# Kernel tuning notes

Measured on AMD Instinct MI355X. Metric: run time of the kernel, lower is better.

The kernel has to match this reference:

```python
import jax, jax.numpy as jnp
import numpy as np

N_NODES = 50000
N_EDGES = 600000
N_MOL = 512
N_ATOM_FEAT = 30   # NUMBER_ATOMIC_GRAPH_FEATURES
N_BOND_FEAT = 10   # NUMBER_BOND_GRAPH_FEATURES


def _sh(v):
    # Real solid spherical harmonics l=0..3, e3nn 'component' normalization
    # (sum_m Y_lm^2 = (2l+1) r^{2l}), normalize=False -> homogeneous polynomials.
    x, y, z = v[..., 0], v[..., 1], v[..., 2]
    r2 = x * x + y * y + z * z
    s3, s5, s15, s105 = 3 ** 0.5, 5 ** 0.5, 15 ** 0.5, 105 ** 0.5
    s70_4, s42_4, s7_2, s105_2 = 70 ** 0.5 / 4, 42 ** 0.5 / 4, 7 ** 0.5 / 2, 105 ** 0.5 / 2
    return jnp.stack([
        jnp.ones_like(x),                                               # l=0
        s3 * x, s3 * y, s3 * z,                                         # l=1
        s15 * x * y, s15 * y * z, 0.5 * s5 * (3 * z * z - r2),
        s15 * x * z, 0.5 * s15 * (x * x - y * y),                       # l=2
        s70_4 * y * (3 * x * x - y * y), s105 * x * y * z,
        s42_4 * y * (5 * z * z - r2), s7_2 * z * (5 * z * z - 3 * r2),
        s42_4 * x * (5 * z * z - r2), s105_2 * z * (x * x - y * y),
        s70_4 * x * (x * x - 3 * y * y),                                # l=3 (no TP path uses it)
    ], axis=-1)


def setup_inputs() -> dict:
    key = jax.random.key(0)
    ks = jax.random.split(key, 12)
    positions = jax.random.normal(ks[0], (N_NODES, 3), jnp.float32)
    x = jax.random.normal(ks[1], (N_NODES, N_ATOM_FEAT), jnp.float32)
    edge_attr = jax.random.normal(ks[2], (N_EDGES, N_BOND_FEAT), jnp.float32)
    edge_src = jax.random.randint(ks[3], (N_EDGES,), 0, N_NODES)
    edge_dst = jax.random.randint(ks[4], (N_EDGES,), 0, N_NODES)
    batch = jnp.sort(jax.random.randint(ks[5], (N_NODES,), 0, N_MOL))
    # tp1: FullyConnectedTensorProduct(30x0e, sh) -> live outputs 64x0e + 24x1o + 16x2e
    W1_0 = jax.random.normal(ks[6], (N_ATOM_FEAT, 64), jnp.float32)
    W1_1 = jax.random.normal(ks[7], (N_ATOM_FEAT, 24), jnp.float32)
    W1_2 = jax.random.normal(ks[8], (N_ATOM_FEAT, 16), jnp.float32)
    # tp2: paths 0e*0e, 1o*1o, 2e*2e -> 1x0e
    W2_0 = jax.random.normal(ks[9], (64,), jnp.float32)
    W2_1 = jax.random.normal(ks[10], (24,), jnp.float32)
    W2_2 = jax.random.normal(ks[11], (16,), jnp.float32)
    return dict(positions=positions, x=x, edge_attr=edge_attr,
                W1_0=W1_0, W1_1=W1_1, W1_2=W1_2,
                W2_0=W2_0, W2_1=W2_1, W2_2=W2_2,
                edge_src=edge_src, edge_dst=edge_dst, batch=batch)


def _forward(positions, x, edge_attr, W1_0, W1_1, W1_2, W2_0, W2_1, W2_2,
             edge_src, edge_dst, batch):
    E = edge_src.shape[0]
    seg = jax.ops.segment_sum
    edge_vec = positions[edge_src] - positions[edge_dst]            # [E,3]
    sh = _sh(edge_vec)                                              # [E,16]
    # mul_edges TP: only bond channel 0 has instructions; path_weight sqrt(2l+1)
    # cancels w3j(0,l,l)=I/sqrt(2l+1) exactly -> plain product.
    ea = edge_attr[:, :1] * sh
    ea0, ea1, ea2 = ea[:, 0:1], ea[:, 1:4], ea[:, 4:9]              # l=3 slice unused (no path)
    deg = seg(jnp.ones((E,), sh.dtype), edge_dst, num_segments=N_NODES)
    inv_sqrt_deg = jnp.where(deg > 0, jax.lax.rsqrt(jnp.maximum(deg, 1.0)), 0.0)[:, None]
    # tp1: 0e x l -> l ; path_weight*w3j collapses to 1/sqrt(fan_in=30)
    W1 = jnp.concatenate([W1_0, W1_1, W1_2], axis=1)                # [30,104]
    a = (x[edge_src] @ W1) * (1.0 / np.sqrt(N_ATOM_FEAT))           # [E,104]
    a0, a1, a2 = a[:, :64], a[:, 64:88], a[:, 88:104]
    e_feat = jnp.concatenate([
        a0 * ea0,                                                   # [E,64]  0e
        (a1[:, :, None] * ea1[:, None, :]).reshape(E, 72),          # [E,24*3] 1o
        (a2[:, :, None] * ea2[:, None, :]).reshape(E, 80),          # [E,16*5] 2e
    ], axis=1)                                                      # [E,216]
    n = seg(e_feat, edge_dst, num_segments=N_NODES) * inv_sqrt_deg  # [N,216]
    # tp2: l x l -> 0e, w3j(l,l,0)=I/sqrt(2l+1), path_weight = 1/sqrt(104)
    g = n[edge_src]                                                 # [E,216]
    t0 = (g[:, :64] * ea0) @ W2_0
    t1 = jnp.einsum('eum,em,u->e', g[:, 64:136].reshape(E, 24, 3), ea1, W2_1)
    t2 = jnp.einsum('eum,em,u->e', g[:, 136:216].reshape(E, 16, 5), ea2, W2_2)
    out_e = (t0 + t1 / np.sqrt(3.0) + t2 / np.sqrt(5.0)) * (1.0 / np.sqrt(104.0))
    node = seg(out_e[:, None], edge_dst, num_segments=N_NODES) * inv_sqrt_deg  # [N,1]
    acc = seg(node, batch, num_segments=N_MOL)                      # [M,1]
    atoms = seg(jnp.ones((N_NODES,), node.dtype), batch, num_segments=N_MOL)[:, None]
    return acc * jnp.where(atoms > 0, jax.lax.rsqrt(jnp.maximum(atoms, 1.0)), 0.0)


def reference(positions, x, edge_attr, W1_0, W1_1, W1_2, W2_0, W2_1, W2_2,
              edge_src, edge_dst, batch):
    return _forward(positions, x, edge_attr, W1_0, W1_1, W1_2,
                    W2_0, W2_1, W2_2, edge_src, edge_dst, batch)
```

## Files before the change

kernel.cpp:

```cpp
#include <hip/hip_runtime.h>

#define DEV_INLINE __device__ __forceinline__
#define MAXDEG 64

static DEV_INLINE void sh_l012(float xx, float yy, float zz, float sh[9]) {
    const float s3  = 1.7320508075688772f;
    const float s5  = 2.23606797749979f;
    const float s15 = 3.872983346207417f;
    float r2 = xx * xx + yy * yy + zz * zz;
    sh[0] = 1.0f;
    sh[1] = s3 * xx;
    sh[2] = s3 * yy;
    sh[3] = s3 * zz;
    sh[4] = s15 * xx * yy;
    sh[5] = s15 * yy * zz;
    sh[6] = 0.5f * s5 * (3.0f * zz * zz - r2);
    sh[7] = s15 * xx * zz;
    sh[8] = 0.5f * s15 * (xx * xx - yy * yy);
}

__global__ void k_prep(const float* __restrict__ x,
                       const float* __restrict__ pos,
                       const float* __restrict__ W1_0, const float* __restrict__ W1_1,
                       const float* __restrict__ W1_2, const float* __restrict__ W2_0,
                       const float* __restrict__ W2_1, const float* __restrict__ W2_2,
                       const int* __restrict__ esrc, const int* __restrict__ edst,
                       const float* __restrict__ eattr, const int* __restrict__ batch,
                       float4* __restrict__ node1, float2* __restrict__ node2,
                       int* __restrict__ deg, int2* __restrict__ rec,
                       int* __restrict__ atoms,
                       int n_nodes, int n_edges) {
    __shared__ float ws[90];
    __shared__ int hist[512];
    int t = threadIdx.x;
    int g = blockIdx.x * blockDim.x + t;
    bool nodeBlock = (blockIdx.x * blockDim.x) < n_nodes;
    if (nodeBlock) {
        const float inv_s30 = 0.18257418583505536f;
        if (t < 30) {
            float s = 0.f;
            for (int u = 0; u < 64; u++) s += W1_0[t * 64 + u] * W2_0[u];
            ws[t] = s * inv_s30;
        } else if (t < 60) {
            int k = t - 30;
            float s = 0.f;
            for (int u = 0; u < 24; u++) s += W1_1[k * 24 + u] * W2_1[u];
            ws[t] = s * inv_s30;
        } else if (t < 90) {
            int k = t - 60;
            float s = 0.f;
            for (int u = 0; u < 16; u++) s += W1_2[k * 16 + u] * W2_2[u];
            ws[t] = s * inv_s30;
        }
        hist[t] = 0;
        hist[t + 256] = 0;
        __syncthreads();
        if (g < n_nodes) {
            const float* xv = x + (size_t)g * 30;
            float s0 = 0.f, s1 = 0.f, s2 = 0.f;
#pragma unroll
            for (int k = 0; k < 30; k++) {
                float xk = xv[k];
                s0 += xk * ws[k];
                s1 += xk * ws[30 + k];
                s2 += xk * ws[60 + k];
            }
            node1[g] = make_float4(pos[g * 3 + 0], pos[g * 3 + 1], pos[g * 3 + 2], s0);
            node2[g] = make_float2(s1, s2);
        }
        int v0 = blockIdx.x * 256;
        int molFirst = batch[min(v0, n_nodes - 1)];
        if (g < n_nodes) atomicAdd(&hist[batch[g] - molFirst], 1);
        __syncthreads();
        int vend = min(v0 + 255, n_nodes - 1);
        int molLast = batch[vend];
        for (int m = t; m <= molLast - molFirst; m += 256)
            if (hist[m] > 0) atomicAdd(atoms + molFirst + m, hist[m]);
    }
    int e = 4 * g;
    if (e + 3 < n_edges) {
        int4 d4 = ((const int4*)edst)[g];
        int4 s4 = ((const int4*)esrc)[g];
        float ea0 = eattr[(size_t)(e + 0) * 10];
        float ea1 = eattr[(size_t)(e + 1) * 10];
        float ea2 = eattr[(size_t)(e + 2) * 10];
        float ea3 = eattr[(size_t)(e + 3) * 10];
        int r0 = atomicAdd(deg + d4.x, 1);
        int r1 = atomicAdd(deg + d4.y, 1);
        int r2 = atomicAdd(deg + d4.z, 1);
        int r3 = atomicAdd(deg + d4.w, 1);
        if (r0 < MAXDEG) rec[d4.x * MAXDEG + r0] = make_int2(s4.x, __float_as_int(ea0));
        if (r1 < MAXDEG) rec[d4.y * MAXDEG + r1] = make_int2(s4.y, __float_as_int(ea1));
        if (r2 < MAXDEG) rec[d4.z * MAXDEG + r2] = make_int2(s4.z, __float_as_int(ea2));
        if (r3 < MAXDEG) rec[d4.w * MAXDEG + r3] = make_int2(s4.w, __float_as_int(ea3));
    } else {
        for (int ee = e; ee < n_edges; ee++) {
            int dst = edst[ee];
            int r = atomicAdd(deg + dst, 1);
            if (r < MAXDEG)
                rec[dst * MAXDEG + r] = make_int2(esrc[ee], __float_as_int(eattr[(size_t)ee * 10]));
        }
    }
}

__global__ void k_passA(const float4* __restrict__ node1, const float2* __restrict__ node2,
                        const int2* __restrict__ rec, const int* __restrict__ deg,
                        float4* __restrict__ Pkg, int n_nodes) {
    int g = blockIdx.x * blockDim.x + threadIdx.x;
    int v = g >> 4, r = g & 15;
    if (v >= n_nodes) return;
    int d = min(deg[v], MAXDEG);
    const int2* row = rec + (size_t)v * MAXDEG;
    float4 pv = node1[v];
    float acc[9];
#pragma unroll
    for (int m = 0; m < 9; m++) acc[m] = 0.f;
    for (int i = r; i < d; i += 16) {
        int2 rcd = row[i];
        int src = rcd.x;
        float ea = __int_as_float(rcd.y);
        float4 n1 = node1[src];
        float2 n2 = node2[src];
        float dx = n1.x - pv.x, dy = n1.y - pv.y, dz = n1.z - pv.z;
        float sh[9];
        sh_l012(dx, dy, dz, sh);
        acc[0] += ea * n1.w;
#pragma unroll
        for (int m = 1; m < 4; m++) acc[m] += ea * sh[m] * n2.x;
#pragma unroll
        for (int m = 4; m < 9; m++) acc[m] += ea * sh[m] * n2.y;
    }
#pragma unroll
    for (int off = 1; off < 16; off <<= 1)
#pragma unroll
        for (int m = 0; m < 9; m++) acc[m] += __shfl_xor(acc[m], off);
    if (r == 0) {
        float s = (d > 0) ? rsqrtf((float)d) : 0.f;
        float4* out = Pkg + (size_t)v * 3;
        out[0] = make_float4(acc[0] * s, acc[1] * s, acc[2] * s, acc[3] * s);
        out[1] = make_float4(acc[4] * s, acc[5] * s, acc[6] * s, acc[7] * s);
        out[2] = make_float4(acc[8] * s, pv.x, pv.y, pv.z);
    }
}

__global__ void k_passB(const float4* __restrict__ node1, const float4* __restrict__ Pkg,
                        const int2* __restrict__ rec, const int* __restrict__ deg,
                        const int* __restrict__ batch, const int* __restrict__ atoms,
                        float* __restrict__ out, int n_nodes) {
    __shared__ float smol[512];
    int t = threadIdx.x;
    smol[t] = 0.f;
    smol[t + 256] = 0.f;
    __syncthreads();
    int g = blockIdx.x * blockDim.x + t;
    int v = g >> 4, r = g & 15;
    int v0 = blockIdx.x * 16;
    const float i3 = 0.5773502691896258f;
    const float i5 = 0.4472135954999579f;
    const float i104 = 0.09805806756909202f;
    int molFirst = batch[min(v0, n_nodes - 1)];
    if (v < n_nodes) {
        int d = min(deg[v], MAXDEG);
        const int2* row = rec + (size_t)v * MAXDEG;
        float4 pv = node1[v];
        float s = 0.f;
        for (int i = r; i < d; i += 16) {
            int2 rcd = row[i];
            int src = rcd.x;
            float ea = __int_as_float(rcd.y);
            const float4* Ps = Pkg + (size_t)src * 3;
            float4 p03 = Ps[0];
            float4 p47 = Ps[1];
            float4 p8p = Ps[2];
            float dx = p8p.y - pv.x, dy = p8p.z - pv.y, dz = p8p.w - pv.z;
            float sh[9];
            sh_l012(dx, dy, dz, sh);
            float t1 = sh[1] * p03.y + sh[2] * p03.z + sh[3] * p03.w;
            float t2 = sh[4] * p47.x + sh[5] * p47.y + sh[6] * p47.z + sh[7] * p47.w + sh[8] * p8p.x;
            s += ea * (p03.x + t1 * i3 + t2 * i5);
        }
#pragma unroll
        for (int off = 1; off < 16; off <<= 1) s += __shfl_xor(s, off);
        if (r == 0) {
            float isd = (d > 0) ? rsqrtf((float)d) : 0.f;
            atomicAdd(&smol[batch[v] - molFirst], s * i104 * isd);
        }
    }
    __syncthreads();
    if (v0 < n_nodes) {
        int vend = min(v0 + 15, n_nodes - 1);
        int nm = batch[vend] - molFirst + 1;
        for (int m = t; m < nm; m += 256) {
            float val = smol[m];
            if (val != 0.f) {
                int a = atoms[molFirst + m];
                float inv = (a > 0) ? rsqrtf((float)a) : 0.f;
                atomicAdd(out + molFirst + m, val * inv);
            }
        }
    }
}

extern "C" void kernel_launch(void* const* d_in, const int* in_sizes, int n_in,
                              void* d_out, int out_size, void* d_ws, size_t ws_size,
                              hipStream_t stream) {
    const float* pos   = (const float*)d_in[0];
    const float* x     = (const float*)d_in[1];
    const float* eattr = (const float*)d_in[2];
    const float* W1_0  = (const float*)d_in[3];
    const float* W1_1  = (const float*)d_in[4];
    const float* W1_2  = (const float*)d_in[5];
    const float* W2_0  = (const float*)d_in[6];
    const float* W2_1  = (const float*)d_in[7];
    const float* W2_2  = (const float*)d_in[8];
    const int* esrc  = (const int*)d_in[9];
    const int* edst  = (const int*)d_in[10];
    const int* batch = (const int*)d_in[11];

    const int n_edges = in_sizes[9];
    const int n_nodes = in_sizes[11];
    const int n_mol   = out_size;
    float* out = (float*)d_out;

    const int BS = 256;
    const int NB = (n_nodes + BS - 1) / BS;
    const int EB4 = (n_edges / 4 + BS - 1) / BS;
    const int VB16 = (16 * n_nodes + BS - 1) / BS;
    const int GRID1 = (EB4 > NB) ? EB4 : NB;

    char* ws = (char*)d_ws;
    size_t off = 0;
    auto carve = [&](size_t bytes) {
        size_t o = off;
        off = (off + bytes + 255) & ~(size_t)255;
        return o;
    };
    size_t off_deg    = carve((size_t)n_nodes * sizeof(int));
    size_t off_atoms  = carve((size_t)n_mol * sizeof(int));
    size_t zero_bytes = off;
    size_t off_n1     = carve((size_t)n_nodes * sizeof(float4));
    size_t off_n2     = carve((size_t)n_nodes * sizeof(float2));
    size_t off_Pkg    = carve((size_t)n_nodes * 3 * sizeof(float4));
    size_t off_rec    = carve((size_t)n_nodes * MAXDEG * sizeof(int2));
    (void)ws_size;

    int*    deg    = (int*)(ws + off_deg);
    int*    atoms  = (int*)(ws + off_atoms);
    float4* node1  = (float4*)(ws + off_n1);
    float2* node2  = (float2*)(ws + off_n2);
    float4* Pkg    = (float4*)(ws + off_Pkg);
    int2*   rec    = (int2*)(ws + off_rec);

    hipMemsetAsync(d_ws, 0, zero_bytes, stream);
    hipMemsetAsync(d_out, 0, (size_t)n_mol * sizeof(float), stream);

    k_prep<<<GRID1, BS, 0, stream>>>(x, pos, W1_0, W1_1, W1_2, W2_0, W2_1, W2_2,
                                     esrc, edst, eattr, batch,
                                     node1, node2, deg, rec, atoms,
                                     n_nodes, n_edges);
    k_passA<<<VB16, BS, 0, stream>>>(node1, node2, rec, deg, Pkg, n_nodes);
    k_passB<<<VB16, BS, 0, stream>>>(node1, Pkg, rec, deg, batch, atoms, out, n_nodes);
}
```

Baseline: 152.9 us.

## Fuse prep and both edge passes into one cooperative kernel with grid syncs

Merges the prep, pass A and pass B kernels, and the two memsets, into a single cooperative kernel. It launches 1024 blocks of 256 threads, and the later phases become grid-stride loops over node chunks. Zeroing of deg, atoms and out moves inside the kernel, and grid-wide barriers replace the kernel boundaries. The goal is to remove launch and memset overhead and the idle gaps between stages. The cost is three grid.sync barriers and a fixed grid size that must fit co-resident on the device, which may also reduce per-phase occupancy.

```diff
diff --git a/kernel.cpp b/kernel.cpp
--- a/kernel.cpp
+++ b/kernel.cpp
@@ -1,4 +1,7 @@
 #include <hip/hip_runtime.h>
+#include <hip/hip_cooperative_groups.h>
+
+namespace cg = cooperative_groups;
 
 #define DEV_INLINE __device__ __forceinline__
 #define MAXDEG 64
@@ -19,21 +22,29 @@
     sh[8] = 0.5f * s15 * (xx * xx - yy * yy);
 }
 
-__global__ void k_prep(const float* __restrict__ x,
-                       const float* __restrict__ pos,
-                       const float* __restrict__ W1_0, const float* __restrict__ W1_1,
-                       const float* __restrict__ W1_2, const float* __restrict__ W2_0,
-                       const float* __restrict__ W2_1, const float* __restrict__ W2_2,
-                       const int* __restrict__ esrc, const int* __restrict__ edst,
-                       const float* __restrict__ eattr, const int* __restrict__ batch,
-                       float4* __restrict__ node1, float2* __restrict__ node2,
-                       int* __restrict__ deg, int2* __restrict__ rec,
-                       int* __restrict__ atoms,
-                       int n_nodes, int n_edges) {
+__global__ void __launch_bounds__(256, 4)
+k_all(const float* __restrict__ x, const float* __restrict__ pos,
+      const float* __restrict__ W1_0, const float* __restrict__ W1_1,
+      const float* __restrict__ W1_2, const float* __restrict__ W2_0,
+      const float* __restrict__ W2_1, const float* __restrict__ W2_2,
+      const int* __restrict__ esrc, const int* __restrict__ edst,
+      const float* __restrict__ eattr, const int* __restrict__ batch,
+      float4* __restrict__ node1, float2* __restrict__ node2,
+      int* __restrict__ deg, int2* __restrict__ rec, int* __restrict__ atoms,
+      float4* __restrict__ Pkg, float* __restrict__ out,
+      int n_nodes, int n_edges, int n_mol) {
+    cg::grid_group grid = cg::this_grid();
     __shared__ float ws[90];
     __shared__ int hist[512];
+    __shared__ float smol[512];
     int t = threadIdx.x;
     int g = blockIdx.x * blockDim.x + t;
+    int nthreads = gridDim.x * blockDim.x;
+
+    for (int i = g; i < n_nodes; i += nthreads) deg[i] = 0;
+    if (g < n_mol) { atoms[g] = 0; out[g] = 0.f; }
+    grid.sync();
+
     bool nodeBlock = (blockIdx.x * blockDim.x) < n_nodes;
     if (nodeBlock) {
         const float inv_s30 = 0.18257418583505536f;
@@ -77,127 +88,129 @@
         for (int m = t; m <= molLast - molFirst; m += 256)
             if (hist[m] > 0) atomicAdd(atoms + molFirst + m, hist[m]);
     }
-    int e = 4 * g;
-    if (e + 3 < n_edges) {
-        int4 d4 = ((const int4*)edst)[g];
-        int4 s4 = ((const int4*)esrc)[g];
-        float ea0 = eattr[(size_t)(e + 0) * 10];
-        float ea1 = eattr[(size_t)(e + 1) * 10];
-        float ea2 = eattr[(size_t)(e + 2) * 10];
-        float ea3 = eattr[(size_t)(e + 3) * 10];
-        int r0 = atomicAdd(deg + d4.x, 1);
-        int r1 = atomicAdd(deg + d4.y, 1);
-        int r2 = atomicAdd(deg + d4.z, 1);
-        int r3 = atomicAdd(deg + d4.w, 1);
-        if (r0 < MAXDEG) rec[d4.x * MAXDEG + r0] = make_int2(s4.x, __float_as_int(ea0));
-        if (r1 < MAXDEG) rec[d4.y * MAXDEG + r1] = make_int2(s4.y, __float_as_int(ea1));
-        if (r2 < MAXDEG) rec[d4.z * MAXDEG + r2] = make_int2(s4.z, __float_as_int(ea2));
-        if (r3 < MAXDEG) rec[d4.w * MAXDEG + r3] = make_int2(s4.w, __float_as_int(ea3));
-    } else {
-        for (int ee = e; ee < n_edges; ee++) {
-            int dst = edst[ee];
-            int r = atomicAdd(deg + dst, 1);
-            if (r < MAXDEG)
-                rec[dst * MAXDEG + r] = make_int2(esrc[ee], __float_as_int(eattr[(size_t)ee * 10]));
-        }
-    }
-}
-
-__global__ void k_passA(const float4* __restrict__ node1, const float2* __restrict__ node2,
-                        const int2* __restrict__ rec, const int* __restrict__ deg,
-                        float4* __restrict__ Pkg, int n_nodes) {
-    int g = blockIdx.x * blockDim.x + threadIdx.x;
-    int v = g >> 4, r = g & 15;
-    if (v >= n_nodes) return;
-    int d = min(deg[v], MAXDEG);
-    const int2* row = rec + (size_t)v * MAXDEG;
-    float4 pv = node1[v];
-    float acc[9];
-#pragma unroll
-    for (int m = 0; m < 9; m++) acc[m] = 0.f;
-    for (int i = r; i < d; i += 16) {
-        int2 rcd = row[i];
-        int src = rcd.x;
-        float ea = __int_as_float(rcd.y);
-        float4 n1 = node1[src];
-        float2 n2 = node2[src];
-        float dx = n1.x - pv.x, dy = n1.y - pv.y, dz = n1.z - pv.z;
-        float sh[9];
-        sh_l012(dx, dy, dz, sh);
-        acc[0] += ea * n1.w;
-#pragma unroll
-        for (int m = 1; m < 4; m++) acc[m] += ea * sh[m] * n2.x;
-#pragma unroll
-        for (int m = 4; m < 9; m++) acc[m] += ea * sh[m] * n2.y;
-    }
-#pragma unroll
-    for (int off = 1; off < 16; off <<= 1)
-#pragma unroll
-        for (int m = 0; m < 9; m++) acc[m] += __shfl_xor(acc[m], off);
-    if (r == 0) {
-        float s = (d > 0) ? rsqrtf((float)d) : 0.f;
-        float4* out = Pkg + (size_t)v * 3;
-        out[0] = make_float4(acc[0] * s, acc[1] * s, acc[2] * s, acc[3] * s);
-        out[1] = make_float4(acc[4] * s, acc[5] * s, acc[6] * s, acc[7] * s);
-        out[2] = make_float4(acc[8] * s, pv.x, pv.y, pv.z);
-    }
-}
-
-__global__ void k_passB(const float4* __restrict__ node1, const float4* __restrict__ Pkg,
-                        const int2* __restrict__ rec, const int* __restrict__ deg,
-                        const int* __restrict__ batch, const int* __restrict__ atoms,
-                        float* __restrict__ out, int n_nodes) {
-    __shared__ float smol[512];
-    int t = threadIdx.x;
-    smol[t] = 0.f;
-    smol[t + 256] = 0.f;
-    __syncthreads();
-    int g = blockIdx.x * blockDim.x + t;
-    int v = g >> 4, r = g & 15;
-    int v0 = blockIdx.x * 16;
+    {
+        int e = 4 * g;
+        if (e + 3 < n_edges) {
+            int4 d4 = ((const int4*)edst)[g];
+            int4 s4 = ((const int4*)esrc)[g];
+            float ea0 = eattr[(size_t)(e + 0) * 10];
+            float ea1 = eattr[(size_t)(e + 1) * 10];
+            float ea2 = eattr[(size_t)(e + 2) * 10];
+            float ea3 = eattr[(size_t)(e + 3) * 10];
+            int r0 = atomicAdd(deg + d4.x, 1);
+            int r1 = atomicAdd(deg + d4.y, 1);
+            int r2 = atomicAdd(deg + d4.z, 1);
+            int r3 = atomicAdd(deg + d4.w, 1);
+            if (r0 < MAXDEG) rec[d4.x * MAXDEG + r0] = make_int2(s4.x, __float_as_int(ea0));
+            if (r1 < MAXDEG) rec[d4.y * MAXDEG + r1] = make_int2(s4.y, __float_as_int(ea1));
+            if (r2 < MAXDEG) rec[d4.z * MAXDEG + r2] = make_int2(s4.z, __float_as_int(ea2));
+            if (r3 < MAXDEG) rec[d4.w * MAXDEG + r3] = make_int2(s4.w, __float_as_int(ea3));
+        } else {
+            for (int ee = e; ee < n_edges; ee++) {
+                int dst = edst[ee];
+                int r = atomicAdd(deg + dst, 1);
+                if (r < MAXDEG)
+                    rec[dst * MAXDEG + r] =
+                        make_int2(esrc[ee], __float_as_int(eattr[(size_t)ee * 10]));
+            }
+        }
+    }
+    grid.sync();
+
+    int nchunk = (16 * n_nodes + 255) / 256;
+    for (int c = blockIdx.x; c < nchunk; c += gridDim.x) {
+        int gg = c * 256 + t;
+        int v = gg >> 4, r = gg & 15;
+        if (v < n_nodes) {
+            int d = min(deg[v], MAXDEG);
+            const int2* row = rec + (size_t)v * MAXDEG;
+            float4 pv = node1[v];
+            float acc[9];
+#pragma unroll
+            for (int m = 0; m < 9; m++) acc[m] = 0.f;
+            for (int i = r; i < d; i += 16) {
+                int2 rcd = row[i];
+                int src = rcd.x;
+                float ea = __int_as_float(rcd.y);
+                float4 n1 = node1[src];
+                float2 n2 = node2[src];
+                float dx = n1.x - pv.x, dy = n1.y - pv.y, dz = n1.z - pv.z;
+                float sh[9];
+                sh_l012(dx, dy, dz, sh);
+                acc[0] += ea * n1.w;
+#pragma unroll
+                for (int m = 1; m < 4; m++) acc[m] += ea * sh[m] * n2.x;
+#pragma unroll
+                for (int m = 4; m < 9; m++) acc[m] += ea * sh[m] * n2.y;
+            }
+#pragma unroll
+            for (int off = 1; off < 16; off <<= 1)
+#pragma unroll
+                for (int m = 0; m < 9; m++) acc[m] += __shfl_xor(acc[m], off);
+            if (r == 0) {
+                float s = (d > 0) ? rsqrtf((float)d) : 0.f;
+                float4* o = Pkg + (size_t)v * 3;
+                o[0] = make_float4(acc[0] * s, acc[1] * s, acc[2] * s, acc[3] * s);
+                o[1] = make_float4(acc[4] * s, acc[5] * s, acc[6] * s, acc[7] * s);
+                o[2] = make_float4(acc[8] * s, pv.x, pv.y, pv.z);
+            }
+        }
+    }
+    grid.sync();
+
     const float i3 = 0.5773502691896258f;
     const float i5 = 0.4472135954999579f;
     const float i104 = 0.09805806756909202f;
-    int molFirst = batch[min(v0, n_nodes - 1)];
-    if (v < n_nodes) {
-        int d = min(deg[v], MAXDEG);
-        const int2* row = rec + (size_t)v * MAXDEG;
-        float4 pv = node1[v];
-        float s = 0.f;
-        for (int i = r; i < d; i += 16) {
-            int2 rcd = row[i];
-            int src = rcd.x;
-            float ea = __int_as_float(rcd.y);
-            const float4* Ps = Pkg + (size_t)src * 3;
-            float4 p03 = Ps[0];
-            float4 p47 = Ps[1];
-            float4 p8p = Ps[2];
-            float dx = p8p.y - pv.x, dy = p8p.z - pv.y, dz = p8p.w - pv.z;
-            float sh[9];
-            sh_l012(dx, dy, dz, sh);
-            float t1 = sh[1] * p03.y + sh[2] * p03.z + sh[3] * p03.w;
-            float t2 = sh[4] * p47.x + sh[5] * p47.y + sh[6] * p47.z + sh[7] * p47.w + sh[8] * p8p.x;
-            s += ea * (p03.x + t1 * i3 + t2 * i5);
-        }
-#pragma unroll
-        for (int off = 1; off < 16; off <<= 1) s += __shfl_xor(s, off);
-        if (r == 0) {
-            float isd = (d > 0) ? rsqrtf((float)d) : 0.f;
-            atomicAdd(&smol[batch[v] - molFirst], s * i104 * isd);
-        }
-    }
-    __syncthreads();
-    if (v0 < n_nodes) {
-        int vend = min(v0 + 15, n_nodes - 1);
-        int nm = batch[vend] - molFirst + 1;
-        for (int m = t; m < nm; m += 256) {
-            float val = smol[m];
-            if (val != 0.f) {
-                int a = atoms[molFirst + m];
-                float inv = (a > 0) ? rsqrtf((float)a) : 0.f;
-                atomicAdd(out + molFirst + m, val * inv);
-            }
-        }
+    for (int c = blockIdx.x; c < nchunk; c += gridDim.x) {
+        smol[t] = 0.f;
+        smol[t + 256] = 0.f;
+        __syncthreads();
+        int gg = c * 256 + t;
+        int v = gg >> 4, r = gg & 15;
+        int v0 = c * 16;
+        int molFirst = batch[min(v0, n_nodes - 1)];
+        if (v < n_nodes) {
+            int d = min(deg[v], MAXDEG);
+            const int2* row = rec + (size_t)v * MAXDEG;
+            float4 pv = node1[v];
+            float s = 0.f;
+            for (int i = r; i < d; i += 16) {
+                int2 rcd = row[i];
+                int src = rcd.x;
+                float ea = __int_as_float(rcd.y);
+                const float4* Ps = Pkg + (size_t)src * 3;
+                float4 p03 = Ps[0];
+                float4 p47 = Ps[1];
+                float4 p8p = Ps[2];
+                float dx = p8p.y - pv.x, dy = p8p.z - pv.y, dz = p8p.w - pv.z;
+                float sh[9];
+                sh_l012(dx, dy, dz, sh);
+                float t1 = sh[1] * p03.y + sh[2] * p03.z + sh[3] * p03.w;
+                float t2 = sh[4] * p47.x + sh[5] * p47.y + sh[6] * p47.z +
+                           sh[7] * p47.w + sh[8] * p8p.x;
+                s += ea * (p03.x + t1 * i3 + t2 * i5);
+            }
+#pragma unroll
+            for (int off = 1; off < 16; off <<= 1) s += __shfl_xor(s, off);
+            if (r == 0) {
+                float isd = (d > 0) ? rsqrtf((float)d) : 0.f;
+                atomicAdd(&smol[batch[v] - molFirst], s * i104 * isd);
+            }
+        }
+        __syncthreads();
+        if (v0 < n_nodes) {
+            int vend = min(v0 + 15, n_nodes - 1);
+            int nm = batch[vend] - molFirst + 1;
+            for (int m = t; m < nm; m += 256) {
+                float val = smol[m];
+                if (val != 0.f) {
+                    int a = atoms[molFirst + m];
+                    float inv = (a > 0) ? rsqrtf((float)a) : 0.f;
+                    atomicAdd(out + molFirst + m, val * inv);
+                }
+            }
+        }
+        __syncthreads();
     }
 }
 
@@ -217,16 +230,10 @@
     const int* edst  = (const int*)d_in[10];
     const int* batch = (const int*)d_in[11];
 
-    const int n_edges = in_sizes[9];
-    const int n_nodes = in_sizes[11];
-    const int n_mol   = out_size;
+    int n_edges = in_sizes[9];
+    int n_nodes = in_sizes[11];
+    int n_mol   = out_size;
     float* out = (float*)d_out;
-
-    const int BS = 256;
-    const int NB = (n_nodes + BS - 1) / BS;
-    const int EB4 = (n_edges / 4 + BS - 1) / BS;
-    const int VB16 = (16 * n_nodes + BS - 1) / BS;
-    const int GRID1 = (EB4 > NB) ? EB4 : NB;
 
     char* ws = (char*)d_ws;
     size_t off = 0;
@@ -235,29 +242,30 @@
         off = (off + bytes + 255) & ~(size_t)255;
         return o;
     };
-    size_t off_deg    = carve((size_t)n_nodes * sizeof(int));
-    size_t off_atoms  = carve((size_t)n_mol * sizeof(int));
-    size_t zero_bytes = off;
-    size_t off_n1     = carve((size_t)n_nodes * sizeof(float4));
-    size_t off_n2     = carve((size_t)n_nodes * sizeof(float2));
-    size_t off_Pkg    = carve((size_t)n_nodes * 3 * sizeof(float4));
-    size_t off_rec    = carve((size_t)n_nodes * MAXDEG * sizeof(int2));
+    size_t off_deg   = carve((size_t)n_nodes * sizeof(int));
+    size_t off_atoms = carve((size_t)n_mol * sizeof(int));
+    size_t off_n1    = carve((size_t)n_nodes * sizeof(float4));
+    size_t off_n2    = carve((size_t)n_nodes * sizeof(float2));
+    size_t off_Pkg   = carve((size_t)n_nodes * 3 * sizeof(float4));
+    size_t off_rec   = carve((size_t)n_nodes * MAXDEG * sizeof(int2));
     (void)ws_size;
 
-    int*    deg    = (int*)(ws + off_deg);
-    int*    atoms  = (int*)(ws + off_atoms);
-    float4* node1  = (float4*)(ws + off_n1);
-    float2* node2  = (float2*)(ws + off_n2);
-    float4* Pkg    = (float4*)(ws + off_Pkg);
-    int2*   rec    = (int2*)(ws + off_rec);
-
-    hipMemsetAsync(d_ws, 0, zero_bytes, stream);
-    hipMemsetAsync(d_out, 0, (size_t)n_mol * sizeof(float), stream);
-
-    k_prep<<<GRID1, BS, 0, stream>>>(x, pos, W1_0, W1_1, W1_2, W2_0, W2_1, W2_2,
-                                     esrc, edst, eattr, batch,
-                                     node1, node2, deg, rec, atoms,
-                                     n_nodes, n_edges);
-    k_passA<<<VB16, BS, 0, stream>>>(node1, node2, rec, deg, Pkg, n_nodes);
-    k_passB<<<VB16, BS, 0, stream>>>(node1, Pkg, rec, deg, batch, atoms, out, n_nodes);
+    int*    deg   = (int*)(ws + off_deg);
+    int*    atoms = (int*)(ws + off_atoms);
+    float4* node1 = (float4*)(ws + off_n1);
+    float2* node2 = (float2*)(ws + off_n2);
+    float4* Pkg   = (float4*)(ws + off_Pkg);
+    int2*   rec   = (int2*)(ws + off_rec);
+
+    void* args[] = {
+        (void*)&x, (void*)&pos,
+        (void*)&W1_0, (void*)&W1_1, (void*)&W1_2,
+        (void*)&W2_0, (void*)&W2_1, (void*)&W2_2,
+        (void*)&esrc, (void*)&edst, (void*)&eattr, (void*)&batch,
+        (void*)&node1, (void*)&node2, (void*)&deg, (void*)&rec, (void*)&atoms,
+        (void*)&Pkg, (void*)&out,
+        (void*)&n_nodes, (void*)&n_edges, (void*)&n_mol,
+    };
+    hipLaunchCooperativeKernel((const void*)k_all, dim3(1024), dim3(256),
+                               args, 0, stream);
 }
```

Result: slower. 458.0 us (+199.6%).
